# Kernel optimization log

Hardware: AMD Instinct MI355X
Metric: run time of the kernel (lower is better)

The kernel has to match this reference:

```python
import jax, jax.numpy as jnp
import numpy as np

B, T, D_IN, D_PROJ = 256, 2048, 25, 128


def setup_inputs() -> dict:
    key = jax.random.key(0)
    ks = jax.random.split(key, 7)
    s1 = 1.0 / np.sqrt(D_IN)
    s2 = 1.0 / np.sqrt(D_PROJ)
    return {
        "x": jax.random.normal(ks[0], (B, T, D_IN), dtype=jnp.float32),
        "ln_gamma": jnp.ones((D_IN,), dtype=jnp.float32),
        "ln_beta": jnp.zeros((D_IN,), dtype=jnp.float32),
        "w1": jax.random.uniform(ks[1], (D_IN, D_PROJ), jnp.float32, -s1, s1),
        "b1": jax.random.uniform(ks[2], (D_PROJ,), jnp.float32, -s1, s1),
        "w2": jax.random.uniform(ks[3], (D_PROJ, D_PROJ), jnp.float32, -s2, s2),
        "b2": jax.random.uniform(ks[4], (D_PROJ,), jnp.float32, -s2, s2),
    }


def reference(x, ln_gamma, ln_beta, w1, b1, w2, b2):
    # LayerNorm over last dim (eps=1e-5, torch default)
    mu = jnp.mean(x, axis=-1, keepdims=True)
    var = jnp.mean(jnp.square(x - mu), axis=-1, keepdims=True)
    xn = (x - mu) * jax.lax.rsqrt(var + 1e-5) * ln_gamma + ln_beta
    h = jnp.einsum("btd,dp->btp", xn, w1) + b1
    h = jax.nn.gelu(h, approximate=False)  # torch nn.GELU default = exact erf
    return jnp.einsum("btp,pq->btq", h, w2) + b2
```

## Files before the change

kernel.cpp:

```cpp
#include <hip/hip_runtime.h>
#include <hip/hip_bf16.h>
#include <stdint.h>

#define BT    (256*2048)
#define DIN   25
#define DP    128
#define MTILE 128
#define NBLK  (BT/MTILE)
#define HSTR  136
#define WREG  (32*HSTR*2)
#define XOFF  4608
#define SM_BYTES (4*WREG)

typedef __attribute__((ext_vector_type(8))) __bf16          bf16x8;
typedef __attribute__((ext_vector_type(4))) float           f32x4;

__device__ __forceinline__ unsigned short f2bf(float f) {
  unsigned int u = __float_as_uint(f);
  u += 0x7fffu + ((u >> 16) & 1u);
  return (unsigned short)(u >> 16);
}

__device__ __forceinline__ float gelu_exact(float x) {
  float z  = 0.70710678118654752f * x;
  float az = __builtin_fabsf(z);
  float t  = __builtin_amdgcn_rcpf(1.0f + 0.3275911f * az);
  float p  = t*(0.254829592f + t*(-0.284496736f + t*(1.421413741f +
             t*(-1.453152027f + t*1.061405429f))));
  float e  = __expf(-z*z);
  float erf_az = 1.0f - p*e;
  float erf_z  = (x < 0.f) ? -erf_az : erf_az;
  return 0.5f * x * (1.0f + erf_z);
}

__device__ __forceinline__ void async16(void* lds, const void* g) {
  __builtin_amdgcn_global_load_lds(
      (const __attribute__((address_space(1))) unsigned int*)g,
      (__attribute__((address_space(3)))       unsigned int*)lds, 16, 0, 0);
}

__global__ void prep_kernel(const float* __restrict__ w1, const float* __restrict__ w2,
                            unsigned short* __restrict__ wf) {
  int idx = blockIdx.x * 256 + threadIdx.x;
  if (idx >= 40 * 512) return;
  int f = idx >> 9, r = idx & 511, l = r >> 3, j = r & 7;
  float val;
  if (f < 8) {
    int k = (l >> 4) * 8 + j;
    int n = f * 16 + (l & 15);
    val = (k < DIN) ? w1[k * DP + n] : 0.f;
  } else {
    int g = f - 8, nt = g >> 2, ks = g & 3;
    int k = ks * 32 + (l >> 4) * 8 + j;
    int n = nt * 16 + (l & 15);
    val = w2[k * DP + n];
  }
  wf[idx] = f2bf(val);
}

__global__ __launch_bounds__(256, 4) void fused_kernel(
    const float* __restrict__ x,   const float* __restrict__ gam,
    const float* __restrict__ bet, const float* __restrict__ b1,
    const float* __restrict__ b2,  const unsigned short* __restrict__ wfr,
    float* __restrict__ out) {
  __shared__ __align__(16) unsigned char smem[SM_BYTES];
  const int tid  = threadIdx.x;
  const int lane = tid & 63, w = tid >> 6;
  const int quad = lane >> 4, l15 = lane & 15;
  const int kbase = quad * 8;
  const long long rowW = (long long)blockIdx.x * MTILE + w * 32;
  unsigned char* wband = smem + w * WREG;
  const unsigned char* wfb = (const unsigned char*)wfr;

  {
    const long long xoff0 = rowW * (DIN * 4);
    const long long xmax  = (long long)BT * DIN * 4 - 16;
#pragma unroll
    for (int i = 0; i < 4; i++) {
      long long off = xoff0 + (long long)(i * 64 + lane) * 16;
      if (off > xmax) off = xmax;
      async16(wband + XOFF + i * 1024 + lane * 16, (const unsigned char*)x + off);
    }
  }

  float gk[8], bk[8];
#pragma unroll
  for (int j = 0; j < 8; j++) {
    int k = kbase + j;
    bool v = (k < DIN);
    gk[j] = v ? gam[k] : 0.f;
    bk[j] = v ? bet[k] : 0.f;
  }
  bf16x8 wb1[8];
#pragma unroll
  for (int nt = 0; nt < 8; nt++)
    wb1[nt] = *(const bf16x8*)(wfb + nt * 1024 + lane * 16);
  float b1v[8];
#pragma unroll
  for (int nt = 0; nt < 8; nt++) b1v[nt] = b1[nt * 16 + l15];

  asm volatile("s_waitcnt vmcnt(0)" ::: "memory");
  __builtin_amdgcn_sched_barrier(0);

  const float* xs = (const float*)(wband + XOFF);
  bf16x8 afrag[2];
#pragma unroll
  for (int t = 0; t < 2; t++) {
    float xv[8];
    float s = 0.f;
#pragma unroll
    for (int j = 0; j < 8; j++) {
      int k = kbase + j;
      float v = 0.f;
      if (k < DIN) v = xs[(t * 16 + l15) * DIN + k];
      xv[j] = v;
      s += v;
    }
    s += __shfl_xor(s, 16);  s += __shfl_xor(s, 32);
    float mu = s * (1.f / DIN);
    float vv = 0.f;
#pragma unroll
    for (int j = 0; j < 8; j++) {
      int k = kbase + j;
      float d = (k < DIN) ? (xv[j] - mu) : 0.f;
      vv += d * d;
    }
    vv += __shfl_xor(vv, 16); vv += __shfl_xor(vv, 32);
    float inv = rsqrtf(vv * (1.f / DIN) + 1e-5f);
    bf16x8 av;
#pragma unroll
    for (int j = 0; j < 8; j++)
      av[j] = (__bf16)((xv[j] - mu) * inv * gk[j] + bk[j]);
    afrag[t] = av;
  }

  __bf16* hbb = (__bf16*)smem;
  const int hrow0 = w * 32;
  const f32x4 zf = {0.f, 0.f, 0.f, 0.f};
  {
    f32x4 acc[8];
#pragma unroll
    for (int nt = 0; nt < 8; nt++)
      acc[nt] = __builtin_amdgcn_mfma_f32_16x16x32_bf16(afrag[0], wb1[nt], zf, 0, 0, 0);
#pragma unroll
    for (int nt = 0; nt < 8; nt++) {
      float bias = b1v[nt];
      int col = nt * 16 + l15;
#pragma unroll
      for (int r = 0; r < 4; r++) {
        int row = hrow0 + quad * 4 + r;
        hbb[row * HSTR + col] = (__bf16)gelu_exact(acc[nt][r] + bias);
      }
    }
  }

  bf16x8 wb2[2][4];
  float bias2[2];
  {
    f32x4 acc[8];
#pragma unroll
    for (int nt = 0; nt < 8; nt++)
      acc[nt] = __builtin_amdgcn_mfma_f32_16x16x32_bf16(afrag[1], wb1[nt], zf, 0, 0, 0);
#pragma unroll
    for (int ni = 0; ni < 2; ni++) {
#pragma unroll
      for (int ks = 0; ks < 4; ks++)
        wb2[ni][ks] = *(const bf16x8*)(wfb + 8192 + (((w * 2 + ni) * 4) + ks) * 1024 + lane * 16);
      bias2[ni] = b2[(w * 2 + ni) * 16 + l15];
    }
#pragma unroll
    for (int nt = 0; nt < 8; nt++) {
      float bias = b1v[nt];
      int col = nt * 16 + l15;
#pragma unroll
      for (int r = 0; r < 4; r++) {
        int row = hrow0 + 16 + quad * 4 + r;
        hbb[row * HSTR + col] = (__bf16)gelu_exact(acc[nt][r] + bias);
      }
    }
  }

  __syncthreads();

  const long long orow0 = (long long)blockIdx.x * MTILE;
  const int c0 = (w * 2 + 0) * 16 + l15;
  const int c1 = (w * 2 + 1) * 16 + l15;
#pragma unroll
  for (int mt = 0; mt < 8; mt++) {
    bf16x8 af[4];
#pragma unroll
    for (int ks = 0; ks < 4; ks++)
      af[ks] = *(const bf16x8*)((const unsigned char*)smem +
                 (mt * 16 + l15) * (HSTR * 2) + ks * 64 + quad * 16);
    f32x4 a0 = zf, a1 = zf;
#pragma unroll
    for (int ks = 0; ks < 4; ks++) {
      a0 = __builtin_amdgcn_mfma_f32_16x16x32_bf16(af[ks], wb2[0][ks], a0, 0, 0, 0);
      a1 = __builtin_amdgcn_mfma_f32_16x16x32_bf16(af[ks], wb2[1][ks], a1, 0, 0, 0);
    }
    float* orow = out + (orow0 + mt * 16) * DP;
#pragma unroll
    for (int r = 0; r < 4; r++) {
      int row = quad * 4 + r;
      orow[row * DP + c0] = a0[r] + bias2[0];
      orow[row * DP + c1] = a1[r] + bias2[1];
    }
  }
}

extern "C" void kernel_launch(void* const* d_in, const int* in_sizes, int n_in,
                              void* d_out, int out_size, void* d_ws, size_t ws_size,
                              hipStream_t stream) {
  const float* x   = (const float*)d_in[0];
  const float* gam = (const float*)d_in[1];
  const float* bet = (const float*)d_in[2];
  const float* w1  = (const float*)d_in[3];
  const float* b1  = (const float*)d_in[4];
  const float* w2  = (const float*)d_in[5];
  const float* b2  = (const float*)d_in[6];
  float* out = (float*)d_out;
  unsigned short* wf = (unsigned short*)d_ws;

  prep_kernel<<<80, 256, 0, stream>>>(w1, w2, wf);
  fused_kernel<<<NBLK, 256, 0, stream>>>(x, gam, bet, b1, b2, wf, out);
}
```

Before: 345.1 us.

## Permute weight columns for vectorized LDS/global stores and XOR-swizzle hidden tile

Weight fragments are reordered in the prep kernel so each lane owns interleaved output columns. GELU results can then be written to LDS as 4-wide bf16 vectors and the final output as float2 stores. The hidden tile now uses an unpadded 256-byte row stride with an XOR swizzle instead of padding to avoid bank conflicts. The x staging load is trimmed to exactly 200 chunks and the occupancy hint is lowered from 4 to 3. The risks are register and LDS pressure changes and a subtle dependency on the swizzle being correct.

New measurement: 328.0 us. 1.05x faster.

```diff
diff --git a/kernel.cpp b/kernel.cpp
--- a/kernel.cpp
+++ b/kernel.cpp
@@ -7,13 +7,14 @@
 #define DP    128
 #define MTILE 128
 #define NBLK  (BT/MTILE)
-#define HSTR  136
-#define WREG  (32*HSTR*2)
-#define XOFF  4608
-#define SM_BYTES (4*WREG)
-
-typedef __attribute__((ext_vector_type(8))) __bf16          bf16x8;
-typedef __attribute__((ext_vector_type(4))) float           f32x4;
+#define BAND  8192
+#define XOFF  4992
+#define SM_BYTES (4*BAND)
+
+typedef __attribute__((ext_vector_type(8))) __bf16 bf16x8;
+typedef __attribute__((ext_vector_type(4))) __bf16 bf16x4;
+typedef __attribute__((ext_vector_type(4))) float  f32x4;
+typedef __attribute__((ext_vector_type(2))) float  f32x2;
 
 __device__ __forceinline__ unsigned short f2bf(float f) {
   unsigned int u = __float_as_uint(f);
@@ -44,21 +45,21 @@
   int idx = blockIdx.x * 256 + threadIdx.x;
   if (idx >= 40 * 512) return;
   int f = idx >> 9, r = idx & 511, l = r >> 3, j = r & 7;
+  int l15 = l & 15, kq = (l >> 4) * 8 + j;
   float val;
   if (f < 8) {
-    int k = (l >> 4) * 8 + j;
-    int n = f * 16 + (l & 15);
-    val = (k < DIN) ? w1[k * DP + n] : 0.f;
+    int n = (f >> 2) * 64 + l15 * 4 + (f & 3);
+    val = (kq < DIN) ? w1[kq * DP + n] : 0.f;
   } else {
-    int g = f - 8, nt = g >> 2, ks = g & 3;
-    int k = ks * 32 + (l >> 4) * 8 + j;
-    int n = nt * 16 + (l & 15);
+    int q = f - 8, F = q >> 2, ks = q & 3;
+    int k = ks * 32 + kq;
+    int n = (F >> 1) * 32 + l15 * 2 + (F & 1);
     val = w2[k * DP + n];
   }
   wf[idx] = f2bf(val);
 }
 
-__global__ __launch_bounds__(256, 4) void fused_kernel(
+__global__ __launch_bounds__(256, 3) void fused_kernel(
     const float* __restrict__ x,   const float* __restrict__ gam,
     const float* __restrict__ bet, const float* __restrict__ b1,
     const float* __restrict__ b2,  const unsigned short* __restrict__ wfr,
@@ -69,18 +70,13 @@
   const int quad = lane >> 4, l15 = lane & 15;
   const int kbase = quad * 8;
   const long long rowW = (long long)blockIdx.x * MTILE + w * 32;
-  unsigned char* wband = smem + w * WREG;
+  unsigned char* band = smem + w * BAND;
   const unsigned char* wfb = (const unsigned char*)wfr;
 
   {
-    const long long xoff0 = rowW * (DIN * 4);
-    const long long xmax  = (long long)BT * DIN * 4 - 16;
-#pragma unroll
-    for (int i = 0; i < 4; i++) {
-      long long off = xoff0 + (long long)(i * 64 + lane) * 16;
-      if (off > xmax) off = xmax;
-      async16(wband + XOFF + i * 1024 + lane * 16, (const unsigned char*)x + off);
-    }
+    const unsigned char* src = (const unsigned char*)x + rowW * (DIN * 4);
+    for (int c = lane; c < 200; c += 64)
+      async16(band + XOFF + c * 16, src + c * 16);
   }
 
   float gk[8], bk[8];
@@ -93,16 +89,17 @@
   }
   bf16x8 wb1[8];
 #pragma unroll
-  for (int nt = 0; nt < 8; nt++)
-    wb1[nt] = *(const bf16x8*)(wfb + nt * 1024 + lane * 16);
+  for (int f = 0; f < 8; f++)
+    wb1[f] = *(const bf16x8*)(wfb + f * 1024 + lane * 16);
   float b1v[8];
 #pragma unroll
-  for (int nt = 0; nt < 8; nt++) b1v[nt] = b1[nt * 16 + l15];
+  for (int f = 0; f < 8; f++)
+    b1v[f] = b1[(f >> 2) * 64 + l15 * 4 + (f & 3)];
 
   asm volatile("s_waitcnt vmcnt(0)" ::: "memory");
   __builtin_amdgcn_sched_barrier(0);
 
-  const float* xs = (const float*)(wband + XOFF);
+  const float* xs = (const float*)(band + XOFF);
   bf16x8 afrag[2];
 #pragma unroll
   for (int t = 0; t < 2; t++) {
@@ -133,77 +130,61 @@
       av[j] = (__bf16)((xv[j] - mu) * inv * gk[j] + bk[j]);
     afrag[t] = av;
   }
-
-  __bf16* hbb = (__bf16*)smem;
-  const int hrow0 = w * 32;
+  asm volatile("s_waitcnt lgkmcnt(0)" ::: "memory");
+  __builtin_amdgcn_sched_barrier(0);
+
   const f32x4 zf = {0.f, 0.f, 0.f, 0.f};
-  {
-    f32x4 acc[8];
-#pragma unroll
-    for (int nt = 0; nt < 8; nt++)
-      acc[nt] = __builtin_amdgcn_mfma_f32_16x16x32_bf16(afrag[0], wb1[nt], zf, 0, 0, 0);
-#pragma unroll
-    for (int nt = 0; nt < 8; nt++) {
-      float bias = b1v[nt];
-      int col = nt * 16 + l15;
+#pragma unroll
+  for (int t = 0; t < 2; t++) {
+#pragma unroll
+    for (int g = 0; g < 2; g++) {
+      f32x4 acc[4];
+#pragma unroll
+      for (int c = 0; c < 4; c++)
+        acc[c] = __builtin_amdgcn_mfma_f32_16x16x32_bf16(afrag[t], wb1[g * 4 + c], zf, 0, 0, 0);
 #pragma unroll
       for (int r = 0; r < 4; r++) {
-        int row = hrow0 + quad * 4 + r;
-        hbb[row * HSTR + col] = (__bf16)gelu_exact(acc[nt][r] + bias);
+        int rl   = t * 16 + quad * 4 + r;
+        int swz  = ((quad * 4 + r) & 7) << 4;
+        bf16x4 hv;
+#pragma unroll
+        for (int c = 0; c < 4; c++)
+          hv[c] = (__bf16)gelu_exact(acc[c][r] + b1v[g * 4 + c]);
+        *(bf16x4*)(band + rl * 256 + ((g * 128 + l15 * 8) ^ swz)) = hv;
       }
     }
   }
 
   bf16x8 wb2[2][4];
-  float bias2[2];
-  {
-    f32x4 acc[8];
-#pragma unroll
-    for (int nt = 0; nt < 8; nt++)
-      acc[nt] = __builtin_amdgcn_mfma_f32_16x16x32_bf16(afrag[1], wb1[nt], zf, 0, 0, 0);
-#pragma unroll
-    for (int ni = 0; ni < 2; ni++) {
-#pragma unroll
-      for (int ks = 0; ks < 4; ks++)
-        wb2[ni][ks] = *(const bf16x8*)(wfb + 8192 + (((w * 2 + ni) * 4) + ks) * 1024 + lane * 16);
-      bias2[ni] = b2[(w * 2 + ni) * 16 + l15];
-    }
-#pragma unroll
-    for (int nt = 0; nt < 8; nt++) {
-      float bias = b1v[nt];
-      int col = nt * 16 + l15;
-#pragma unroll
-      for (int r = 0; r < 4; r++) {
-        int row = hrow0 + 16 + quad * 4 + r;
-        hbb[row * HSTR + col] = (__bf16)gelu_exact(acc[nt][r] + bias);
-      }
-    }
-  }
+#pragma unroll
+  for (int ni = 0; ni < 2; ni++)
+#pragma unroll
+    for (int ks = 0; ks < 4; ks++)
+      wb2[ni][ks] = *(const bf16x8*)(wfb + 8192 + (((w * 2 + ni) * 4) + ks) * 1024 + lane * 16);
+  f32x2 bias2 = *(const f32x2*)(b2 + w * 32 + 2 * l15);
 
   __syncthreads();
 
   const long long orow0 = (long long)blockIdx.x * MTILE;
-  const int c0 = (w * 2 + 0) * 16 + l15;
-  const int c1 = (w * 2 + 1) * 16 + l15;
+  const int rswz = (l15 & 7) << 4;
 #pragma unroll
   for (int mt = 0; mt < 8; mt++) {
     bf16x8 af[4];
 #pragma unroll
     for (int ks = 0; ks < 4; ks++)
-      af[ks] = *(const bf16x8*)((const unsigned char*)smem +
-                 (mt * 16 + l15) * (HSTR * 2) + ks * 64 + quad * 16);
+      af[ks] = *(const bf16x8*)(smem + (mt * 16 + l15) * 256 + ((ks * 64 + quad * 16) ^ rswz));
     f32x4 a0 = zf, a1 = zf;
 #pragma unroll
     for (int ks = 0; ks < 4; ks++) {
       a0 = __builtin_amdgcn_mfma_f32_16x16x32_bf16(af[ks], wb2[0][ks], a0, 0, 0, 0);
       a1 = __builtin_amdgcn_mfma_f32_16x16x32_bf16(af[ks], wb2[1][ks], a1, 0, 0, 0);
     }
-    float* orow = out + (orow0 + mt * 16) * DP;
+    float* orow = out + (orow0 + mt * 16) * DP + w * 32 + 2 * l15;
 #pragma unroll
     for (int r = 0; r < 4; r++) {
       int row = quad * 4 + r;
-      orow[row * DP + c0] = a0[r] + bias2[0];
-      orow[row * DP + c1] = a1[r] + bias2[1];
+      f32x2 o; o[0] = a0[r] + bias2[0]; o[1] = a1[r] + bias2[1];
+      *(f32x2*)(orow + row * DP) = o;
     }
   }
 }
```
